# Optimization experiments

Hardware: AMD Instinct MI355X
Metric: run time of the kernel (lower is better)

Reference implementation:

```python
import jax, jax.numpy as jnp
import numpy as np

B, T, F, H, V = 16, 512, 512, 2048, 64
INPUT_INT_SCALE = 3.0
INT16_MIN, INT16_MAX = -32768, 32767


def setup_inputs() -> dict:
    key = jax.random.key(0)
    ks = jax.random.split(key, 8)
    x = jax.random.normal(ks[0], (B, T, F), dtype=jnp.float32)
    # int4 weights stored as int32 in [-8, 7]
    W_res_i4 = jax.random.randint(ks[1], (H, H), -8, 8, dtype=jnp.int32)
    W_in_i4 = jax.random.randint(ks[2], (H, F), -8, 8, dtype=jnp.int32)
    # per-row quantization scales (positive)
    S_res_row = jax.random.uniform(ks[3], (H,), dtype=jnp.float32, minval=0.01, maxval=0.2)
    S_in_row = jax.random.uniform(ks[4], (H,), dtype=jnp.float32, minval=0.01, maxval=0.2)
    g_res = jnp.float32(1.0)
    g_in = jnp.float32(1.0)
    W_out_w = jax.random.normal(ks[5], (V, H), dtype=jnp.float32) / np.float32(np.sqrt(H))
    W_out_b = jnp.zeros((V,), dtype=jnp.float32)
    return {
        "x": x, "S_res_row": S_res_row, "S_in_row": S_in_row,
        "g_res": g_res, "g_in": g_in,
        "W_out_w": W_out_w, "W_out_b": W_out_b,
        "W_res_i4": W_res_i4, "W_in_i4": W_in_i4,
    }


def reference(x, S_res_row, S_in_row, g_res, g_in, W_out_w, W_out_b, W_res_i4, W_in_i4):
    # row scales (matches _row_scales)
    s_res = (S_res_row / 49.0 * g_res)[None, :]                     # (1,H)
    s_in = (S_in_row / (7.0 * max(1.0, INPUT_INT_SCALE)) * g_in)[None, :]  # (1,H)

    def step(h, x_t):
        # quantize input frame and hidden state to integers (detached in torch)
        u_int = jax.lax.stop_gradient(jnp.round(x_t * INPUT_INT_SCALE)).astype(jnp.int32)     # (B,F)
        h_int = jax.lax.stop_gradient(jnp.round(jnp.clip(h, -1.0, 1.0) * 7.0)).astype(jnp.int32)  # (B,H)
        # integer matvecs: y[b,k] = sum_j W[k,j] * v[b,j]
        out_res = jnp.einsum('bh,kh->bk', h_int, W_res_i4)  # (B,H) int32
        out_in = jnp.einsum('bf,kf->bk', u_int, W_in_i4)    # (B,H) int32
        # int16 saturation, then row scale + gain, tanh
        out_res_f = jnp.clip(out_res, INT16_MIN, INT16_MAX).astype(jnp.float32)
        out_in_f = jnp.clip(out_in, INT16_MIN, INT16_MAX).astype(jnp.float32)
        h_new = jnp.tanh(out_res_f * s_res + out_in_f * s_in)
        return h_new, h_new

    h0 = jnp.zeros((x.shape[0], W_res_i4.shape[0]), dtype=jnp.float32)
    _, Hs = jax.lax.scan(step, h0, jnp.swapaxes(x, 0, 1))  # (T,B,H)
    Hs = jnp.swapaxes(Hs, 0, 1)                            # (B,T,H)
    # readout
    return jnp.einsum('bth,vh->btv', Hs, W_out_w) + W_out_b
```

## Files before the change

### kernel.cpp

```cpp
#include <hip/hip_runtime.h>
#include <hip/hip_bf16.h>


#define B_ 16
#define T_ 512
#define F_ 512
#define H_ 2048
#define V_ 64
#define SLICES 16
#define RPW 128
#define NTHREADS 256
#define NWG 256

#if defined(__has_builtin)
#if __has_builtin(__builtin_amdgcn_sdot8)
#define HAVE_SDOT8 1
#endif
#endif

__device__ __forceinline__ int sdot8(int a, int b, int c) {
#ifdef HAVE_SDOT8
  return __builtin_amdgcn_sdot8(a, b, c, false);
#else
#pragma unroll
  for (int i = 0; i < 8; ++i) {
    int av = (a << (28 - 4 * i)) >> 28;
    int bv = (b << (28 - 4 * i)) >> 28;
    c += av * bv;
  }
  return c;
#endif
}

__device__ __forceinline__ float tanh_ref(float x) {
  float ax = fabsf(x);
  float xc = fminf(fmaxf(x, -7.90531110763549805f), 7.90531110763549805f);
  float x2 = __fmul_rn(xc, xc);
  float p = -2.76076847742355e-16f;
  p = __fmaf_rn(x2, p, 2.00018790482477e-13f);
  p = __fmaf_rn(x2, p, -8.60467152213735e-11f);
  p = __fmaf_rn(x2, p, 5.12229709037114e-08f);
  p = __fmaf_rn(x2, p, 1.48572235717979e-05f);
  p = __fmaf_rn(x2, p, 6.37261928875436e-04f);
  p = __fmaf_rn(x2, p, 4.89352455891786e-03f);
  p = __fmul_rn(xc, p);
  float q = 1.19825839466702e-06f;
  q = __fmaf_rn(x2, q, 1.18534705686654e-04f);
  q = __fmaf_rn(x2, q, 2.26843463243900e-03f);
  q = __fmaf_rn(x2, q, 4.89352518554385e-03f);
  float r = __fdiv_rn(p, q);
  return (ax < 0.0004f) ? x : r;
}

__device__ __forceinline__ unsigned f2bf(float f) {
  unsigned u = __float_as_uint(f);
  return (u + 0x7fffu + ((u >> 16) & 1u)) >> 16;
}

__device__ __forceinline__ unsigned poll_tag(const unsigned long long* p, unsigned tag) {
  unsigned long long u;
  do {
    u = __hip_atomic_load(p, __ATOMIC_RELAXED, __HIP_MEMORY_SCOPE_AGENT);
  } while ((unsigned)(u >> 32) != tag);
  return (unsigned)u;
}

__device__ __forceinline__ void publish_tag(unsigned long long* p, unsigned data, unsigned tag) {
  unsigned long long u = ((unsigned long long)tag << 32) | data;
  __hip_atomic_store(p, u, __ATOMIC_RELAXED, __HIP_MEMORY_SCOPE_AGENT);
}

__global__ void pack_weights(const int* __restrict__ Wres, const int* __restrict__ Win,
                             int* __restrict__ wr4, int* __restrict__ wi4) {
  int id = blockIdx.x * blockDim.x + threadIdx.x;
  if (id < H_ * 256) {
    const int* src = Wres + id * 8;
    int pk = 0;
#pragma unroll
    for (int i = 0; i < 8; ++i) pk |= (src[i] & 15) << (4 * i);
    wr4[id] = pk;
  } else {
    int id2 = id - H_ * 256;
    if (id2 < H_ * 64) {
      const int* src = Win + id2 * 8;
      int pk = 0;
#pragma unroll
      for (int i = 0; i < 8; ++i) pk |= (src[i] & 15) << (4 * i);
      wi4[id2] = pk;
    }
  }
}

__global__ void pack_u(const float* __restrict__ x, int* __restrict__ um, int* __restrict__ ua) {
  int idx = blockIdx.x * blockDim.x + threadIdx.x;
  if (idx >= B_ * T_ * 64) return;
  const float* src = x + (size_t)idx * 8;
  int pm = 0, pa = 0;
#pragma unroll
  for (int i = 0; i < 8; ++i) {
    int u = (int)rintf(__fmul_rn(src[i], 3.0f));
    int vv = u + 128;
    pm |= (vv & 7) << (4 * i);
    pa |= (((vv >> 3) - 16) & 15) << (4 * i);
  }
  um[idx] = pm;
  ua[idx] = pa;
}

__global__ void __launch_bounds__(NTHREADS, 1) esn_main(
    const int* __restrict__ um, const int* __restrict__ ua,
    const int* __restrict__ wr4, const int* __restrict__ wi4,
    unsigned long long* hq2,
    const float* __restrict__ S_res, const float* __restrict__ S_in,
    const float* __restrict__ g_res, const float* __restrict__ g_in,
    unsigned* __restrict__ Hs, int t0, int t1) {
  extern __shared__ char smem[];
  ::int4* lw4 = (::int4*)smem;
  int* lds_h4 = (int*)(lw4 + 8192);
  int* lds_um = lds_h4 + 256;
  int* lds_ua = lds_um + 64;

  const int wg = blockIdx.x;
  const int b = wg & 15, slice = wg >> 4;
  const int tid = threadIdx.x;
  const unsigned lane = tid & 63;
  const int wave = tid >> 6;
  const int half = tid & 1;
  const int grow = slice * RPW + (tid >> 1);

  {
    const ::int4* gw = (const ::int4*)wr4;
#pragma unroll 4
    for (int m = 0; m < 32; ++m) lw4[m * 256 + tid] = gw[grow * 64 + half * 32 + m];
  }
  ::int4 rwm[8];
  {
    const ::int4* gwi = (const ::int4*)wi4;
#pragma unroll
    for (int m = 0; m < 8; ++m) rwm[m] = gwi[grow * 16 + half * 8 + m];
  }
  const float sr = __fmul_rn(__fdiv_rn(S_res[grow], 49.0f), g_res[0]);
  const float si = __fmul_rn(__fdiv_rn(S_in[grow], 21.0f), g_in[0]);

  const ::int4* lh4 = (const ::int4*)lds_h4 + half * 32;
  const ::int4* lum4 = (const ::int4*)lds_um + half * 8;
  const ::int4* lua4 = (const ::int4*)lds_ua + half * 8;

  unsigned ureg = 0;
  if (tid < 64)
    ureg = um[(b * T_ + t0) * 64 + tid];
  else if (tid < 128)
    ureg = ua[(b * T_ + t0) * 64 + (tid - 64)];

  for (int t = t0; t < t1; ++t) {
    const int cur = t & 1, nxt = cur ^ 1;
    if (tid < 64)
      lds_um[tid] = ureg;
    else if (tid < 128)
      lds_ua[tid - 64] = ureg;
    __syncthreads();

    unsigned unext = 0;
    if (t + 1 < t1) {
      if (tid < 64)
        unext = um[(b * T_ + t + 1) * 64 + tid];
      else if (tid < 128)
        unext = ua[(b * T_ + t + 1) * 64 + (tid - 64)];
    }

    int am = 0, aa = 0;
#pragma unroll
    for (int m = 0; m < 8; ++m) {
      ::int4 w = rwm[m];
      ::int4 uM = lum4[m];
      ::int4 uA = lua4[m];
      am = sdot8(w.x, uM.x, am); am = sdot8(w.y, uM.y, am);
      am = sdot8(w.z, uM.z, am); am = sdot8(w.w, uM.w, am);
      aa = sdot8(w.x, uA.x, aa); aa = sdot8(w.y, uA.y, aa);
      aa = sdot8(w.z, uA.z, aa); aa = sdot8(w.w, uA.w, aa);
    }
    int accin = am + (aa << 3);
    accin += __shfl_xor(accin, 1);

    unsigned hd = poll_tag(hq2 + ((size_t)(cur * 16 + b) * 256 + tid), (unsigned)t);
    lds_h4[tid] = (int)hd;
    __syncthreads();

    int c0 = 0, c1 = 0, c2 = 0, c3 = 0;
#pragma unroll
    for (int m = 0; m < 32; m += 4) {
      ::int4 w0 = lw4[(m + 0) * 256 + tid];
      ::int4 w1 = lw4[(m + 1) * 256 + tid];
      ::int4 w2 = lw4[(m + 2) * 256 + tid];
      ::int4 w3 = lw4[(m + 3) * 256 + tid];
      ::int4 h0 = lh4[m + 0];
      ::int4 h1 = lh4[m + 1];
      ::int4 h2 = lh4[m + 2];
      ::int4 h3 = lh4[m + 3];
      c0 = sdot8(w0.x, h0.x, c0); c0 = sdot8(w0.y, h0.y, c0);
      c0 = sdot8(w0.z, h0.z, c0); c0 = sdot8(w0.w, h0.w, c0);
      c1 = sdot8(w1.x, h1.x, c1); c1 = sdot8(w1.y, h1.y, c1);
      c1 = sdot8(w1.z, h1.z, c1); c1 = sdot8(w1.w, h1.w, c1);
      c2 = sdot8(w2.x, h2.x, c2); c2 = sdot8(w2.y, h2.y, c2);
      c2 = sdot8(w2.z, h2.z, c2); c2 = sdot8(w2.w, h2.w, c2);
      c3 = sdot8(w3.x, h3.x, c3); c3 = sdot8(w3.y, h3.y, c3);
      c3 = sdot8(w3.z, h3.z, c3); c3 = sdot8(w3.w, h3.w, c3);
    }
    int acc = (c0 + c1) + (c2 + c3);
    acc += __shfl_xor(acc, 1);

    int cr = min(max(acc, -32768), 32767);
    int ci = min(max(accin, -32768), 32767);
    float arg = __fadd_rn(__fmul_rn((float)cr, sr), __fmul_rn((float)ci, si));
    float hn = tanh_ref(arg);
    float hc = fminf(fmaxf(hn, -1.0f), 1.0f);
    int qv = (int)rintf(__fmul_rn(hc, 7.0f));

    unsigned nib = ((unsigned)qv & 15u) << (4 * ((lane >> 1) & 7));
    nib |= (unsigned)__shfl_xor((int)nib, 1);
    nib |= (unsigned)__shfl_xor((int)nib, 2);
    nib |= (unsigned)__shfl_xor((int)nib, 4);
    nib |= (unsigned)__shfl_xor((int)nib, 8);
    if ((lane & 15) == 0)
      publish_tag(hq2 + ((size_t)(nxt * 16 + b) * 256 + slice * 16 + wave * 4 + (lane >> 4)),
                  nib, (unsigned)(t + 1));

    unsigned bfb = f2bf(hn);
    unsigned other = (unsigned)__shfl_xor((int)bfb, 2);
    if ((tid & 3) == 0)
      Hs[(size_t)(b * T_ + t) * (H_ / 2) + slice * 64 + (tid >> 2)] = bfb | (other << 16);

    ureg = unext;
  }
}

#define ACC8(acc, p, w0, w1)                                    \
  acc = fmaf(__uint_as_float(p.x << 16), w0.x, acc);            \
  acc = fmaf(__uint_as_float(p.x & 0xffff0000u), w0.y, acc);    \
  acc = fmaf(__uint_as_float(p.y << 16), w0.z, acc);            \
  acc = fmaf(__uint_as_float(p.y & 0xffff0000u), w0.w, acc);    \
  acc = fmaf(__uint_as_float(p.z << 16), w1.x, acc);            \
  acc = fmaf(__uint_as_float(p.z & 0xffff0000u), w1.y, acc);    \
  acc = fmaf(__uint_as_float(p.w << 16), w1.z, acc);            \
  acc = fmaf(__uint_as_float(p.w & 0xffff0000u), w1.w, acc);

__global__ void __launch_bounds__(256) readout(const unsigned* __restrict__ Hs,
                                               const float* __restrict__ Wout,
                                               const float* __restrict__ Wb,
                                               float* __restrict__ out) {
  const int v = threadIdx.x & 63;
  const int rg = threadIdx.x >> 6;
  const int bt0 = blockIdx.x * 16 + rg * 4;
  const float* wrow = Wout + (size_t)v * H_;
  const unsigned* h0 = Hs + (size_t)bt0 * (H_ / 2);
  float a0 = Wb[v], a1 = a0, a2 = a0, a3 = a0;
  for (int j = 0; j < H_ / 2; j += 4) {
    float4 w0 = *(const float4*)(wrow + 2 * j);
    float4 w1 = *(const float4*)(wrow + 2 * j + 4);
    uint4 p0 = *(const uint4*)(h0 + j);
    uint4 p1 = *(const uint4*)(h0 + (H_ / 2) + j);
    uint4 p2 = *(const uint4*)(h0 + 2 * (H_ / 2) + j);
    uint4 p3 = *(const uint4*)(h0 + 3 * (H_ / 2) + j);
    ACC8(a0, p0, w0, w1)
    ACC8(a1, p1, w0, w1)
    ACC8(a2, p2, w0, w1)
    ACC8(a3, p3, w0, w1)
  }
  out[(size_t)(bt0 + 0) * V_ + v] = a0;
  out[(size_t)(bt0 + 1) * V_ + v] = a1;
  out[(size_t)(bt0 + 2) * V_ + v] = a2;
  out[(size_t)(bt0 + 3) * V_ + v] = a3;
}

extern "C" void kernel_launch(void* const* d_in, const int* in_sizes, int n_in,
                              void* d_out, int out_size, void* d_ws, size_t ws_size,
                              hipStream_t stream) {
  const float* x = (const float*)d_in[0];
  const float* S_res = (const float*)d_in[1];
  const float* S_in = (const float*)d_in[2];
  const float* g_res = (const float*)d_in[3];
  const float* g_in = (const float*)d_in[4];
  const float* Woutw = (const float*)d_in[5];
  const float* Woutb = (const float*)d_in[6];
  const int* Wres = (const int*)d_in[7];
  const int* Win = (const int*)d_in[8];

  char* ws = (char*)d_ws;
  unsigned long long* hq2 = (unsigned long long*)(ws + 4096);
  int* um = (int*)(ws + (1 << 20));
  int* ua = um + (1 << 19);
  int* wr4 = ua + (1 << 19);
  int* wi4 = wr4 + (1 << 19);
  unsigned* Hs = (unsigned*)(ws + (8 << 20));

  hipMemsetAsync(d_ws, 0, 4096 + 65536, stream);
  hipLaunchKernelGGL(pack_weights, dim3(2560), dim3(256), 0, stream, Wres, Win, wr4, wi4);
  hipLaunchKernelGGL(pack_u, dim3(2048), dim3(256), 0, stream, x, um, ua);

  const int smem_bytes = 131072 + 1536;
  (void)hipFuncSetAttribute((const void*)esn_main, hipFuncAttributeMaxDynamicSharedMemorySize,
                            smem_bytes);

  float* outf = (float*)d_out;
  int t0 = 0, t1 = T_;
  void* args[] = {&um, &ua, &wr4, &wi4, &hq2, &S_res, &S_in,
                  &g_res, &g_in, &Hs, &t0, &t1};
  hipError_t e = hipLaunchCooperativeKernel((const void*)esn_main, dim3(NWG), dim3(NTHREADS),
                                            args, smem_bytes, stream);
  if (e != hipSuccess) {
    for (int t = 0; t < T_; ++t) {
      hipLaunchKernelGGL(esn_main, dim3(NWG), dim3(NTHREADS), smem_bytes, stream,
                         um, ua, wr4, wi4, hq2, S_res, S_in, g_res, g_in, Hs, t, t + 1);
    }
  }
  hipLaunchKernelGGL(readout, dim3(B_ * T_ / 16), dim3(256), 0, stream,
                     Hs, Woutw, Woutb, outf);
}
```

Measured before the change: 1.118 ms.

## Split recurrent matvec across 512 workgroups with four threads per row

Raises the workgroup count from 256 to 512, so each block owns 64 hidden rows and four threads share a row (quarter-K each), halving per-block LDS weight footprint and allowing two blocks per CU. The hidden-state poll is now done by one wave reading four tagged words per lane with s_sleep backoff, written into a padded, double-buffered LDS array, which removes one barrier per step. Weight LDS reads are issued early via inline asm ds_read_b128 before the poll so they overlap the wait, and the next input frame is prefetched two steps ahead. The cost is more blocks polling and publishing through global memory per step, plus extra shuffle reductions.

```diff
diff --git a/kernel.cpp b/kernel.cpp
--- a/kernel.cpp
+++ b/kernel.cpp
@@ -7,10 +7,12 @@
 #define F_ 512
 #define H_ 2048
 #define V_ 64
-#define SLICES 16
-#define RPW 128
+#define SLICES 32
+#define RPW 64
 #define NTHREADS 256
-#define NWG 256
+#define NWG 512
+
+typedef int i4v __attribute__((ext_vector_type(4)));
 
 #if defined(__has_builtin)
 #if __has_builtin(__builtin_amdgcn_sdot8)
@@ -57,14 +59,6 @@
   return (u + 0x7fffu + ((u >> 16) & 1u)) >> 16;
 }
 
-__device__ __forceinline__ unsigned poll_tag(const unsigned long long* p, unsigned tag) {
-  unsigned long long u;
-  do {
-    u = __hip_atomic_load(p, __ATOMIC_RELAXED, __HIP_MEMORY_SCOPE_AGENT);
-  } while ((unsigned)(u >> 32) != tag);
-  return (unsigned)u;
-}
-
 __device__ __forceinline__ void publish_tag(unsigned long long* p, unsigned data, unsigned tag) {
   unsigned long long u = ((unsigned long long)tag << 32) | data;
   __hip_atomic_store(p, u, __ATOMIC_RELAXED, __HIP_MEMORY_SCOPE_AGENT);
@@ -107,107 +101,127 @@
   ua[idx] = pa;
 }
 
-__global__ void __launch_bounds__(NTHREADS, 1) esn_main(
+#define WLD(i, OFFSTR) \
+  asm volatile("ds_read_b128 %0, %1 offset:" OFFSTR : "=v"(wreg[i]) : "v"(lds_wb))
+
+__global__ void __launch_bounds__(NTHREADS, 2) esn_main(
     const int* __restrict__ um, const int* __restrict__ ua,
     const int* __restrict__ wr4, const int* __restrict__ wi4,
     unsigned long long* hq2,
     const float* __restrict__ S_res, const float* __restrict__ S_in,
     const float* __restrict__ g_res, const float* __restrict__ g_in,
     unsigned* __restrict__ Hs, int t0, int t1) {
-  extern __shared__ char smem[];
+  extern __shared__ __align__(16) char smem[];
   ::int4* lw4 = (::int4*)smem;
-  int* lds_h4 = (int*)(lw4 + 8192);
-  int* lds_um = lds_h4 + 256;
-  int* lds_ua = lds_um + 64;
+  int* lds_h = (int*)(lw4 + 16 * 256);
+  int* lds_u = lds_h + 2 * 272;
 
   const int wg = blockIdx.x;
   const int b = wg & 15, slice = wg >> 4;
   const int tid = threadIdx.x;
   const unsigned lane = tid & 63;
-  const int wave = tid >> 6;
-  const int half = tid & 1;
-  const int grow = slice * RPW + (tid >> 1);
+  const int q = tid & 3;
+  const int grow = slice * RPW + (tid >> 2);
 
   {
     const ::int4* gw = (const ::int4*)wr4;
 #pragma unroll 4
-    for (int m = 0; m < 32; ++m) lw4[m * 256 + tid] = gw[grow * 64 + half * 32 + m];
-  }
-  ::int4 rwm[8];
+    for (int m = 0; m < 16; ++m) lw4[m * 256 + tid] = gw[grow * 64 + q * 16 + m];
+  }
+  ::int4 rwm[4];
   {
     const ::int4* gwi = (const ::int4*)wi4;
 #pragma unroll
-    for (int m = 0; m < 8; ++m) rwm[m] = gwi[grow * 16 + half * 8 + m];
+    for (int m = 0; m < 4; ++m) rwm[m] = gwi[grow * 16 + q * 4 + m];
   }
   const float sr = __fmul_rn(__fdiv_rn(S_res[grow], 49.0f), g_res[0]);
   const float si = __fmul_rn(__fdiv_rn(S_in[grow], 21.0f), g_in[0]);
 
-  const ::int4* lh4 = (const ::int4*)lds_h4 + half * 32;
-  const ::int4* lum4 = (const ::int4*)lds_um + half * 8;
-  const ::int4* lua4 = (const ::int4*)lds_ua + half * 8;
+  const unsigned lds_wb = (unsigned)(size_t)smem + (unsigned)tid * 16u;
 
   unsigned ureg = 0;
-  if (tid < 64)
-    ureg = um[(b * T_ + t0) * 64 + tid];
-  else if (tid < 128)
-    ureg = ua[(b * T_ + t0) * 64 + (tid - 64)];
+  if (tid < 128) {
+    unsigned v0 = (tid < 64) ? (unsigned)um[(b * T_ + t0) * 64 + tid]
+                             : (unsigned)ua[(b * T_ + t0) * 64 + (tid - 64)];
+    lds_u[(t0 & 1) * 128 + tid] = (int)v0;
+    if (t0 + 1 < T_)
+      ureg = (tid < 64) ? (unsigned)um[(b * T_ + t0 + 1) * 64 + tid]
+                        : (unsigned)ua[(b * T_ + t0 + 1) * 64 + (tid - 64)];
+  }
+  __syncthreads();
 
   for (int t = t0; t < t1; ++t) {
-    const int cur = t & 1, nxt = cur ^ 1;
-    if (tid < 64)
-      lds_um[tid] = ureg;
-    else if (tid < 128)
-      lds_ua[tid - 64] = ureg;
-    __syncthreads();
-
-    unsigned unext = 0;
-    if (t + 1 < t1) {
-      if (tid < 64)
-        unext = um[(b * T_ + t + 1) * 64 + tid];
-      else if (tid < 128)
-        unext = ua[(b * T_ + t + 1) * 64 + (tid - 64)];
-    }
+    const int cbuf = t & 1, nbuf = cbuf ^ 1;
+    if (t + 1 < t1 && tid < 128) lds_u[nbuf * 128 + tid] = (int)ureg;
 
     int am = 0, aa = 0;
-#pragma unroll
-    for (int m = 0; m < 8; ++m) {
-      ::int4 w = rwm[m];
-      ::int4 uM = lum4[m];
-      ::int4 uA = lua4[m];
-      am = sdot8(w.x, uM.x, am); am = sdot8(w.y, uM.y, am);
-      am = sdot8(w.z, uM.z, am); am = sdot8(w.w, uM.w, am);
-      aa = sdot8(w.x, uA.x, aa); aa = sdot8(w.y, uA.y, aa);
-      aa = sdot8(w.z, uA.z, aa); aa = sdot8(w.w, uA.w, aa);
+    {
+      const ::int4* lu = (const ::int4*)(lds_u + cbuf * 128);
+#pragma unroll
+      for (int m = 0; m < 4; ++m) {
+        ::int4 w = rwm[m];
+        ::int4 uM = lu[q * 4 + m];
+        ::int4 uA = lu[16 + q * 4 + m];
+        am = sdot8(w.x, uM.x, am); am = sdot8(w.y, uM.y, am);
+        am = sdot8(w.z, uM.z, am); am = sdot8(w.w, uM.w, am);
+        aa = sdot8(w.x, uA.x, aa); aa = sdot8(w.y, uA.y, aa);
+        aa = sdot8(w.z, uA.z, aa); aa = sdot8(w.w, uA.w, aa);
+      }
     }
     int accin = am + (aa << 3);
     accin += __shfl_xor(accin, 1);
-
-    unsigned hd = poll_tag(hq2 + ((size_t)(cur * 16 + b) * 256 + tid), (unsigned)t);
-    lds_h4[tid] = (int)hd;
+    accin += __shfl_xor(accin, 2);
+
+    i4v wreg[16];
+    WLD(0, "0");      WLD(1, "4096");   WLD(2, "8192");   WLD(3, "12288");
+    WLD(4, "16384");  WLD(5, "20480");  WLD(6, "24576");  WLD(7, "28672");
+    WLD(8, "32768");  WLD(9, "36864");  WLD(10, "40960"); WLD(11, "45056");
+    WLD(12, "49152"); WLD(13, "53248"); WLD(14, "57344"); WLD(15, "61440");
+
+    if (tid < 64) {
+      const unsigned long long* p = hq2 + (size_t)(cbuf * 16 + b) * 256 + tid * 4;
+      unsigned long long u0, u1, u2, u3;
+      const unsigned tag = (unsigned)t;
+      for (;;) {
+        u0 = __hip_atomic_load(p + 0, __ATOMIC_RELAXED, __HIP_MEMORY_SCOPE_AGENT);
+        u1 = __hip_atomic_load(p + 1, __ATOMIC_RELAXED, __HIP_MEMORY_SCOPE_AGENT);
+        u2 = __hip_atomic_load(p + 2, __ATOMIC_RELAXED, __HIP_MEMORY_SCOPE_AGENT);
+        u3 = __hip_atomic_load(p + 3, __ATOMIC_RELAXED, __HIP_MEMORY_SCOPE_AGENT);
+        unsigned d = ((unsigned)(u0 >> 32) ^ tag) | ((unsigned)(u1 >> 32) ^ tag) |
+                     ((unsigned)(u2 >> 32) ^ tag) | ((unsigned)(u3 >> 32) ^ tag);
+        if (d == 0) break;
+        __builtin_amdgcn_s_sleep(1);
+      }
+      ::int4 hv;
+      hv.x = (int)u0; hv.y = (int)u1; hv.z = (int)u2; hv.w = (int)u3;
+      ((::int4*)(lds_h + cbuf * 272))[(tid >> 4) * 17 + (tid & 15)] = hv;
+    }
+
     __syncthreads();
+    __builtin_amdgcn_sched_barrier(0);
 
     int c0 = 0, c1 = 0, c2 = 0, c3 = 0;
-#pragma unroll
-    for (int m = 0; m < 32; m += 4) {
-      ::int4 w0 = lw4[(m + 0) * 256 + tid];
-      ::int4 w1 = lw4[(m + 1) * 256 + tid];
-      ::int4 w2 = lw4[(m + 2) * 256 + tid];
-      ::int4 w3 = lw4[(m + 3) * 256 + tid];
-      ::int4 h0 = lh4[m + 0];
-      ::int4 h1 = lh4[m + 1];
-      ::int4 h2 = lh4[m + 2];
-      ::int4 h3 = lh4[m + 3];
-      c0 = sdot8(w0.x, h0.x, c0); c0 = sdot8(w0.y, h0.y, c0);
-      c0 = sdot8(w0.z, h0.z, c0); c0 = sdot8(w0.w, h0.w, c0);
-      c1 = sdot8(w1.x, h1.x, c1); c1 = sdot8(w1.y, h1.y, c1);
-      c1 = sdot8(w1.z, h1.z, c1); c1 = sdot8(w1.w, h1.w, c1);
-      c2 = sdot8(w2.x, h2.x, c2); c2 = sdot8(w2.y, h2.y, c2);
-      c2 = sdot8(w2.z, h2.z, c2); c2 = sdot8(w2.w, h2.w, c2);
-      c3 = sdot8(w3.x, h3.x, c3); c3 = sdot8(w3.y, h3.y, c3);
-      c3 = sdot8(w3.z, h3.z, c3); c3 = sdot8(w3.w, h3.w, c3);
+    {
+      const ::int4* lh = (const ::int4*)(lds_h + cbuf * 272);
+#pragma unroll
+      for (int m = 0; m < 16; m += 4) {
+        ::int4 h0 = lh[q * 17 + m + 0];
+        ::int4 h1 = lh[q * 17 + m + 1];
+        ::int4 h2 = lh[q * 17 + m + 2];
+        ::int4 h3 = lh[q * 17 + m + 3];
+        c0 = sdot8(wreg[m + 0].x, h0.x, c0); c0 = sdot8(wreg[m + 0].y, h0.y, c0);
+        c0 = sdot8(wreg[m + 0].z, h0.z, c0); c0 = sdot8(wreg[m + 0].w, h0.w, c0);
+        c1 = sdot8(wreg[m + 1].x, h1.x, c1); c1 = sdot8(wreg[m + 1].y, h1.y, c1);
+        c1 = sdot8(wreg[m + 1].z, h1.z, c1); c1 = sdot8(wreg[m + 1].w, h1.w, c1);
+        c2 = sdot8(wreg[m + 2].x, h2.x, c2); c2 = sdot8(wreg[m + 2].y, h2.y, c2);
+        c2 = sdot8(wreg[m + 2].z, h2.z, c2); c2 = sdot8(wreg[m + 2].w, h2.w, c2);
+        c3 = sdot8(wreg[m + 3].x, h3.x, c3); c3 = sdot8(wreg[m + 3].y, h3.y, c3);
+        c3 = sdot8(wreg[m + 3].z, h3.z, c3); c3 = sdot8(wreg[m + 3].w, h3.w, c3);
+      }
     }
     int acc = (c0 + c1) + (c2 + c3);
     acc += __shfl_xor(acc, 1);
+    acc += __shfl_xor(acc, 2);
 
     int cr = min(max(acc, -32768), 32767);
     int ci = min(max(accin, -32768), 32767);
@@ -216,21 +230,22 @@
     float hc = fminf(fmaxf(hn, -1.0f), 1.0f);
     int qv = (int)rintf(__fmul_rn(hc, 7.0f));
 
-    unsigned nib = ((unsigned)qv & 15u) << (4 * ((lane >> 1) & 7));
-    nib |= (unsigned)__shfl_xor((int)nib, 1);
-    nib |= (unsigned)__shfl_xor((int)nib, 2);
+    unsigned nib = ((unsigned)qv & 15u) << (4 * ((lane >> 2) & 7));
     nib |= (unsigned)__shfl_xor((int)nib, 4);
     nib |= (unsigned)__shfl_xor((int)nib, 8);
-    if ((lane & 15) == 0)
-      publish_tag(hq2 + ((size_t)(nxt * 16 + b) * 256 + slice * 16 + wave * 4 + (lane >> 4)),
+    nib |= (unsigned)__shfl_xor((int)nib, 16);
+    if ((lane & 31) == 0)
+      publish_tag(hq2 + (size_t)((t ^ 1) & 1) * 0 +
+                      (size_t)(nbuf * 16 + b) * 256 + slice * 8 + (tid >> 6) * 2 + (lane >> 5),
                   nib, (unsigned)(t + 1));
 
     unsigned bfb = f2bf(hn);
-    unsigned other = (unsigned)__shfl_xor((int)bfb, 2);
-    if ((tid & 3) == 0)
-      Hs[(size_t)(b * T_ + t) * (H_ / 2) + slice * 64 + (tid >> 2)] = bfb | (other << 16);
-
-    ureg = unext;
+    unsigned other = (unsigned)__shfl_xor((int)bfb, 4);
+    if ((tid & 7) == 0)
+      Hs[(size_t)(b * T_ + t) * (H_ / 2) + slice * 32 + (tid >> 3)] = bfb | (other << 16);
+    if (t + 2 < T_ && tid < 128)
+      ureg = (tid < 64) ? (unsigned)um[(b * T_ + t + 2) * 64 + tid]
+                        : (unsigned)ua[(b * T_ + t + 2) * 64 + (tid - 64)];
   }
 }
 
@@ -297,11 +312,10 @@
   hipLaunchKernelGGL(pack_weights, dim3(2560), dim3(256), 0, stream, Wres, Win, wr4, wi4);
   hipLaunchKernelGGL(pack_u, dim3(2048), dim3(256), 0, stream, x, um, ua);
 
-  const int smem_bytes = 131072 + 1536;
+  const int smem_bytes = 65536 + 2 * 272 * 4 + 2 * 128 * 4;
   (void)hipFuncSetAttribute((const void*)esn_main, hipFuncAttributeMaxDynamicSharedMemorySize,
                             smem_bytes);
 
-  float* outf = (float*)d_out;
   int t0 = 0, t1 = T_;
   void* args[] = {&um, &ua, &wr4, &wi4, &hq2, &S_res, &S_in,
                   &g_res, &g_in, &Hs, &t0, &t1};
@@ -314,5 +328,5 @@
     }
   }
   hipLaunchKernelGGL(readout, dim3(B_ * T_ / 16), dim3(256), 0, stream,
-                     Hs, Woutw, Woutb, outf);
-}
+                     Hs, Woutw, Woutb, (float*)d_out);
+}
```

After: 1.040 ms. 1.07x faster.

## Hoist input projection into batched GEMM and restructure recurrence with replicated flags

Applied to the files above, without the earlier changes.

Computes the input projection for all timesteps in a separate parallel kernel before the recurrence, removing it from the serial critical path. The recurrent kernel is reorganized so each workgroup owns 8 rows across all batches. Each wave handles one batch per step and keeps its weights in registers instead of LDS. Hidden-state nibbles are published to REP replicated flag buffers to spread polling contention, and the next steps' flag loads are software-prefetched so the pipeline runs four steps deep. This adds an fp32 intermediate buffer of B*T*H and a multi-copy store per step.

```diff
diff --git a/kernel.cpp b/kernel.cpp
--- a/kernel.cpp
+++ b/kernel.cpp
@@ -7,10 +7,11 @@
 #define F_ 512
 #define H_ 2048
 #define V_ 64
-#define SLICES 16
-#define RPW 128
-#define NTHREADS 256
 #define NWG 256
+#define NTHREADS 128
+#define REP 8
+
+typedef unsigned long long ull;
 
 #if defined(__has_builtin)
 #if __has_builtin(__builtin_amdgcn_sdot8)
@@ -57,17 +58,11 @@
   return (u + 0x7fffu + ((u >> 16) & 1u)) >> 16;
 }
 
-__device__ __forceinline__ unsigned poll_tag(const unsigned long long* p, unsigned tag) {
-  unsigned long long u;
-  do {
-    u = __hip_atomic_load(p, __ATOMIC_RELAXED, __HIP_MEMORY_SCOPE_AGENT);
-  } while ((unsigned)(u >> 32) != tag);
-  return (unsigned)u;
-}
-
-__device__ __forceinline__ void publish_tag(unsigned long long* p, unsigned data, unsigned tag) {
-  unsigned long long u = ((unsigned long long)tag << 32) | data;
-  __hip_atomic_store(p, u, __ATOMIC_RELAXED, __HIP_MEMORY_SCOPE_AGENT);
+__device__ __forceinline__ ull xld(const ull* p) {
+  return __hip_atomic_load(p, __ATOMIC_RELAXED, __HIP_MEMORY_SCOPE_AGENT);
+}
+__device__ __forceinline__ void xst(ull* p, ull v) {
+  __hip_atomic_store(p, v, __ATOMIC_RELAXED, __HIP_MEMORY_SCOPE_AGENT);
 }
 
 __global__ void pack_weights(const int* __restrict__ Wres, const int* __restrict__ Win,
@@ -107,131 +102,158 @@
   ua[idx] = pa;
 }
 
+__global__ void __launch_bounds__(256) input_gemm(
+    const int* __restrict__ um, const int* __restrict__ ua, const int* __restrict__ wi4,
+    const float* __restrict__ S_in, const float* __restrict__ g_in, float* __restrict__ fin) {
+  __shared__ int su[1024];
+  const int btg = blockIdx.x;
+  const int row = blockIdx.y * 256 + threadIdx.x;
+  for (int k = threadIdx.x; k < 1024; k += 256) {
+    int bt = k >> 7, c = k & 127;
+    su[k] = (c < 64) ? um[(btg * 8 + bt) * 64 + c] : ua[(btg * 8 + bt) * 64 + (c - 64)];
+  }
+  __syncthreads();
+  ::int4 w[16];
+  const ::int4* gw = (const ::int4*)wi4;
+#pragma unroll
+  for (int i = 0; i < 16; ++i) w[i] = gw[row * 16 + i];
+  const float si = __fmul_rn(__fdiv_rn(S_in[row], 21.0f), g_in[0]);
+#pragma unroll
+  for (int g = 0; g < 8; ++g) {
+    const ::int4* uM = (const ::int4*)(su + g * 128);
+    const ::int4* uA = (const ::int4*)(su + g * 128 + 64);
+    int am = 0, aa = 0;
+#pragma unroll
+    for (int i = 0; i < 16; ++i) {
+      ::int4 wi = w[i]; ::int4 m = uM[i]; ::int4 a = uA[i];
+      am = sdot8(wi.x, m.x, am); am = sdot8(wi.y, m.y, am);
+      am = sdot8(wi.z, m.z, am); am = sdot8(wi.w, m.w, am);
+      aa = sdot8(wi.x, a.x, aa); aa = sdot8(wi.y, a.y, aa);
+      aa = sdot8(wi.z, a.z, aa); aa = sdot8(wi.w, a.w, aa);
+    }
+    int acc = am + (aa << 3);
+    acc = min(max(acc, -32768), 32767);
+    fin[(size_t)(btg * 8 + g) * H_ + row] = __fmul_rn((float)acc, si);
+  }
+}
+
 __global__ void __launch_bounds__(NTHREADS, 1) esn_main(
-    const int* __restrict__ um, const int* __restrict__ ua,
-    const int* __restrict__ wr4, const int* __restrict__ wi4,
-    unsigned long long* hq2,
-    const float* __restrict__ S_res, const float* __restrict__ S_in,
-    const float* __restrict__ g_res, const float* __restrict__ g_in,
-    unsigned* __restrict__ Hs, int t0, int t1) {
-  extern __shared__ char smem[];
-  ::int4* lw4 = (::int4*)smem;
-  int* lds_h4 = (int*)(lw4 + 8192);
-  int* lds_um = lds_h4 + 256;
-  int* lds_ua = lds_um + 64;
-
+    const int* __restrict__ wr4, ull* hq,
+    const float* __restrict__ S_res, const float* __restrict__ g_res,
+    const float* __restrict__ fin, unsigned* __restrict__ Hs, int t0, int t1) {
+  __shared__ int lds_h[2][320];
   const int wg = blockIdx.x;
-  const int b = wg & 15, slice = wg >> 4;
   const int tid = threadIdx.x;
-  const unsigned lane = tid & 63;
-  const int wave = tid >> 6;
-  const int half = tid & 1;
-  const int grow = slice * RPW + (tid >> 1);
-
+  const int wv = tid >> 6;
+  const int lane = tid & 63;
+  const int r = lane >> 3, kq = lane & 7;
+  const int grow = wg * 8 + r;
+  const size_t cpy = (size_t)(wg & (REP - 1));
+  int* hb = lds_h[wv];
+  const int wofs = (lane >> 2) * 20 + (lane & 3) * 4;
+  int* hrd = hb + 40 * kq;
+
+  ::int4 wreg[8];
   {
     const ::int4* gw = (const ::int4*)wr4;
-#pragma unroll 4
-    for (int m = 0; m < 32; ++m) lw4[m * 256 + tid] = gw[grow * 64 + half * 32 + m];
-  }
-  ::int4 rwm[8];
-  {
-    const ::int4* gwi = (const ::int4*)wi4;
-#pragma unroll
-    for (int m = 0; m < 8; ++m) rwm[m] = gwi[grow * 16 + half * 8 + m];
+#pragma unroll
+    for (int j = 0; j < 8; ++j) wreg[j] = gw[grow * 64 + kq * 8 + j];
   }
   const float sr = __fmul_rn(__fdiv_rn(S_res[grow], 49.0f), g_res[0]);
-  const float si = __fmul_rn(__fdiv_rn(S_in[grow], 21.0f), g_in[0]);
-
-  const ::int4* lh4 = (const ::int4*)lds_h4 + half * 32;
-  const ::int4* lum4 = (const ::int4*)lds_um + half * 8;
-  const ::int4* lua4 = (const ::int4*)lds_ua + half * 8;
-
-  unsigned ureg = 0;
-  if (tid < 64)
-    ureg = um[(b * T_ + t0) * 64 + tid];
-  else if (tid < 128)
-    ureg = ua[(b * T_ + t0) * 64 + (tid - 64)];
-
-  for (int t = t0; t < t1; ++t) {
-    const int cur = t & 1, nxt = cur ^ 1;
-    if (tid < 64)
-      lds_um[tid] = ureg;
-    else if (tid < 128)
-      lds_ua[tid - 64] = ureg;
-    __syncthreads();
-
-    unsigned unext = 0;
-    if (t + 1 < t1) {
-      if (tid < 64)
-        unext = um[(b * T_ + t + 1) * 64 + tid];
-      else if (tid < 128)
-        unext = ua[(b * T_ + t + 1) * 64 + (tid - 64)];
-    }
-
-    int am = 0, aa = 0;
-#pragma unroll
-    for (int m = 0; m < 8; ++m) {
-      ::int4 w = rwm[m];
-      ::int4 uM = lum4[m];
-      ::int4 uA = lua4[m];
-      am = sdot8(w.x, uM.x, am); am = sdot8(w.y, uM.y, am);
-      am = sdot8(w.z, uM.z, am); am = sdot8(w.w, uM.w, am);
-      aa = sdot8(w.x, uA.x, aa); aa = sdot8(w.y, uA.y, aa);
-      aa = sdot8(w.z, uA.z, aa); aa = sdot8(w.w, uA.w, aa);
-    }
-    int accin = am + (aa << 3);
-    accin += __shfl_xor(accin, 1);
-
-    unsigned hd = poll_tag(hq2 + ((size_t)(cur * 16 + b) * 256 + tid), (unsigned)t);
-    lds_h4[tid] = (int)hd;
-    __syncthreads();
-
-    int c0 = 0, c1 = 0, c2 = 0, c3 = 0;
-#pragma unroll
-    for (int m = 0; m < 32; m += 4) {
-      ::int4 w0 = lw4[(m + 0) * 256 + tid];
-      ::int4 w1 = lw4[(m + 1) * 256 + tid];
-      ::int4 w2 = lw4[(m + 2) * 256 + tid];
-      ::int4 w3 = lw4[(m + 3) * 256 + tid];
-      ::int4 h0 = lh4[m + 0];
-      ::int4 h1 = lh4[m + 1];
-      ::int4 h2 = lh4[m + 2];
-      ::int4 h3 = lh4[m + 3];
-      c0 = sdot8(w0.x, h0.x, c0); c0 = sdot8(w0.y, h0.y, c0);
-      c0 = sdot8(w0.z, h0.z, c0); c0 = sdot8(w0.w, h0.w, c0);
-      c1 = sdot8(w1.x, h1.x, c1); c1 = sdot8(w1.y, h1.y, c1);
-      c1 = sdot8(w1.z, h1.z, c1); c1 = sdot8(w1.w, h1.w, c1);
-      c2 = sdot8(w2.x, h2.x, c2); c2 = sdot8(w2.y, h2.y, c2);
-      c2 = sdot8(w2.z, h2.z, c2); c2 = sdot8(w2.w, h2.w, c2);
-      c3 = sdot8(w3.x, h3.x, c3); c3 = sdot8(w3.y, h3.y, c3);
-      c3 = sdot8(w3.z, h3.z, c3); c3 = sdot8(w3.w, h3.w, c3);
-    }
-    int acc = (c0 + c1) + (c2 + c3);
-    acc += __shfl_xor(acc, 1);
-
-    int cr = min(max(acc, -32768), 32767);
-    int ci = min(max(accin, -32768), 32767);
-    float arg = __fadd_rn(__fmul_rn((float)cr, sr), __fmul_rn((float)ci, si));
-    float hn = tanh_ref(arg);
-    float hc = fminf(fmaxf(hn, -1.0f), 1.0f);
-    int qv = (int)rintf(__fmul_rn(hc, 7.0f));
-
-    unsigned nib = ((unsigned)qv & 15u) << (4 * ((lane >> 1) & 7));
-    nib |= (unsigned)__shfl_xor((int)nib, 1);
-    nib |= (unsigned)__shfl_xor((int)nib, 2);
-    nib |= (unsigned)__shfl_xor((int)nib, 4);
-    nib |= (unsigned)__shfl_xor((int)nib, 8);
-    if ((lane & 15) == 0)
-      publish_tag(hq2 + ((size_t)(nxt * 16 + b) * 256 + slice * 16 + wave * 4 + (lane >> 4)),
-                  nib, (unsigned)(t + 1));
-
-    unsigned bfb = f2bf(hn);
-    unsigned other = (unsigned)__shfl_xor((int)bfb, 2);
-    if ((tid & 3) == 0)
-      Hs[(size_t)(b * T_ + t) * (H_ / 2) + slice * 64 + (tid >> 2)] = bfb | (other << 16);
-
-    ureg = unext;
-  }
+
+  const int sBeg = t0 * 8, sEnd = t1 * 8;
+
+#define PRE(P, sarg)                                                                     \
+  {                                                                                      \
+    int sc_ = (sarg);                                                                    \
+    if (sc_ > sEnd - 1) sc_ = sEnd - 1;                                                  \
+    const int tt_ = sc_ >> 3, bb_ = ((sc_ & 7) << 1) | wv;                               \
+    const ull* pp_ = hq + (((cpy << 5) + ((size_t)(tt_ & 1) << 4) + bb_) << 8) + (lane << 2); \
+    P##a = xld(pp_); P##b = xld(pp_ + 1); P##c = xld(pp_ + 2); P##d = xld(pp_ + 3);      \
+    P##f = fin[((((size_t)bb_ << 9) + tt_) << 11) + grow];                               \
+  }
+
+#define CONS(P, sarg)                                                                    \
+  {                                                                                      \
+    const int s_ = (sarg);                                                               \
+    const int tt = s_ >> 3;                                                              \
+    const int bb = ((s_ & 7) << 1) | wv;                                                 \
+    const unsigned tg = (unsigned)tt;                                                    \
+    const ull* pp = hq + (((cpy << 5) + ((size_t)(tt & 1) << 4) + bb) << 8) + (lane << 2); \
+    while ((((unsigned)(P##a >> 32)) ^ tg) | (((unsigned)(P##b >> 32)) ^ tg) |           \
+           (((unsigned)(P##c >> 32)) ^ tg) | (((unsigned)(P##d >> 32)) ^ tg)) {          \
+      P##a = xld(pp); P##b = xld(pp + 1); P##c = xld(pp + 2); P##d = xld(pp + 3);        \
+    }                                                                                    \
+    ::int4 hv_;                                                                          \
+    hv_.x = (int)P##a; hv_.y = (int)P##b; hv_.z = (int)P##c; hv_.w = (int)P##d;          \
+    const float finv = P##f;                                                             \
+    PRE(P, s_ + 4);                                                                      \
+    *(::int4*)(hb + wofs) = hv_;                                                         \
+    __builtin_amdgcn_sched_barrier(0);                                                   \
+    int c0 = 0, c1 = 0, c2 = 0, c3 = 0;                                                  \
+    {                                                                                    \
+      ::int4 h0 = *(const ::int4*)(hrd + 0);  ::int4 h1 = *(const ::int4*)(hrd + 4);     \
+      ::int4 h2 = *(const ::int4*)(hrd + 8);  ::int4 h3 = *(const ::int4*)(hrd + 12);    \
+      ::int4 h4 = *(const ::int4*)(hrd + 20); ::int4 h5 = *(const ::int4*)(hrd + 24);    \
+      ::int4 h6 = *(const ::int4*)(hrd + 28); ::int4 h7 = *(const ::int4*)(hrd + 32);    \
+      c0 = sdot8(wreg[0].x, h0.x, c0); c0 = sdot8(wreg[0].y, h0.y, c0);                  \
+      c0 = sdot8(wreg[0].z, h0.z, c0); c0 = sdot8(wreg[0].w, h0.w, c0);                  \
+      c1 = sdot8(wreg[1].x, h1.x, c1); c1 = sdot8(wreg[1].y, h1.y, c1);                  \
+      c1 = sdot8(wreg[1].z, h1.z, c1); c1 = sdot8(wreg[1].w, h1.w, c1);                  \
+      c2 = sdot8(wreg[2].x, h2.x, c2); c2 = sdot8(wreg[2].y, h2.y, c2);                  \
+      c2 = sdot8(wreg[2].z, h2.z, c2); c2 = sdot8(wreg[2].w, h2.w, c2);                  \
+      c3 = sdot8(wreg[3].x, h3.x, c3); c3 = sdot8(wreg[3].y, h3.y, c3);                  \
+      c3 = sdot8(wreg[3].z, h3.z, c3); c3 = sdot8(wreg[3].w, h3.w, c3);                  \
+      c0 = sdot8(wreg[4].x, h4.x, c0); c0 = sdot8(wreg[4].y, h4.y, c0);                  \
+      c0 = sdot8(wreg[4].z, h4.z, c0); c0 = sdot8(wreg[4].w, h4.w, c0);                  \
+      c1 = sdot8(wreg[5].x, h5.x, c1); c1 = sdot8(wreg[5].y, h5.y, c1);                  \
+      c1 = sdot8(wreg[5].z, h5.z, c1); c1 = sdot8(wreg[5].w, h5.w, c1);                  \
+      c2 = sdot8(wreg[6].x, h6.x, c2); c2 = sdot8(wreg[6].y, h6.y, c2);                  \
+      c2 = sdot8(wreg[6].z, h6.z, c2); c2 = sdot8(wreg[6].w, h6.w, c2);                  \
+      c3 = sdot8(wreg[7].x, h7.x, c3); c3 = sdot8(wreg[7].y, h7.y, c3);                  \
+      c3 = sdot8(wreg[7].z, h7.z, c3); c3 = sdot8(wreg[7].w, h7.w, c3);                  \
+    }                                                                                    \
+    int acc = (c0 + c1) + (c2 + c3);                                                     \
+    acc += __shfl_xor(acc, 1);                                                           \
+    acc += __shfl_xor(acc, 2);                                                           \
+    acc += __shfl_xor(acc, 4);                                                           \
+    int cr = min(max(acc, -32768), 32767);                                               \
+    float arg = __fadd_rn(__fmul_rn((float)cr, sr), finv);                               \
+    float hn = tanh_ref(arg);                                                            \
+    float hc = fminf(fmaxf(hn, -1.0f), 1.0f);                                            \
+    int qv = (int)rintf(__fmul_rn(hc, 7.0f));                                            \
+    unsigned nib = ((unsigned)qv & 15u) << (4 * r);                                      \
+    nib |= (unsigned)__shfl_xor((int)nib, 8);                                            \
+    nib |= (unsigned)__shfl_xor((int)nib, 16);                                           \
+    nib |= (unsigned)__shfl_xor((int)nib, 32);                                           \
+    if (lane == 0) {                                                                     \
+      ull uv = ((ull)(unsigned)(tt + 1) << 32) | nib;                                    \
+      ull* pb = hq + ((((size_t)((tt + 1) & 1) << 4) + bb) << 8) + wg;                   \
+      _Pragma("unroll")                                                                  \
+      for (int c_ = 0; c_ < REP; ++c_) xst(pb + ((size_t)c_ << 13), uv);                 \
+    }                                                                                    \
+    unsigned bfb = f2bf(hn);                                                             \
+    unsigned oth = (unsigned)__shfl_xor((int)bfb, 8);                                    \
+    if ((lane & 15) == 0)                                                                \
+      Hs[((((size_t)bb << 9) + tt) << 10) + wg * 4 + (lane >> 4)] = bfb | (oth << 16);   \
+  }
+
+  ull p0a, p0b, p0c, p0d; float p0f;
+  ull p1a, p1b, p1c, p1d; float p1f;
+  ull p2a, p2b, p2c, p2d; float p2f;
+  ull p3a, p3b, p3c, p3d; float p3f;
+  PRE(p0, sBeg)
+  PRE(p1, sBeg + 1)
+  PRE(p2, sBeg + 2)
+  PRE(p3, sBeg + 3)
+  for (int s = sBeg; s < sEnd; s += 4) {
+    CONS(p0, s)
+    CONS(p1, s + 1)
+    CONS(p2, s + 2)
+    CONS(p3, s + 3)
+  }
+#undef PRE
+#undef CONS
 }
 
 #define ACC8(acc, p, w0, w1)                                    \
@@ -286,33 +308,30 @@
   const int* Win = (const int*)d_in[8];
 
   char* ws = (char*)d_ws;
-  unsigned long long* hq2 = (unsigned long long*)(ws + 4096);
-  int* um = (int*)(ws + (1 << 20));
-  int* ua = um + (1 << 19);
-  int* wr4 = ua + (1 << 19);
-  int* wi4 = wr4 + (1 << 19);
-  unsigned* Hs = (unsigned*)(ws + (8 << 20));
-
-  hipMemsetAsync(d_ws, 0, 4096 + 65536, stream);
+  ull* hq = (ull*)ws;
+  int* wr4 = (int*)(ws + (1 << 20));
+  int* wi4 = (int*)(ws + (3 << 20));
+  int* um = (int*)(ws + ((size_t)4 << 20));
+  int* ua = (int*)(ws + ((size_t)6 << 20));
+  unsigned* Hs = (unsigned*)(ws + ((size_t)8 << 20));
+  float* fin = (float*)(ws + ((size_t)40 << 20));
+
+  hipMemsetAsync(hq, 0, (size_t)REP * 32 * 256 * 8, stream);
   hipLaunchKernelGGL(pack_weights, dim3(2560), dim3(256), 0, stream, Wres, Win, wr4, wi4);
   hipLaunchKernelGGL(pack_u, dim3(2048), dim3(256), 0, stream, x, um, ua);
-
-  const int smem_bytes = 131072 + 1536;
-  (void)hipFuncSetAttribute((const void*)esn_main, hipFuncAttributeMaxDynamicSharedMemorySize,
-                            smem_bytes);
-
-  float* outf = (float*)d_out;
+  hipLaunchKernelGGL(input_gemm, dim3(B_ * T_ / 8, 8), dim3(256), 0, stream,
+                     um, ua, wi4, S_in, g_in, fin);
+
   int t0 = 0, t1 = T_;
-  void* args[] = {&um, &ua, &wr4, &wi4, &hq2, &S_res, &S_in,
-                  &g_res, &g_in, &Hs, &t0, &t1};
+  void* args[] = {&wr4, &hq, &S_res, &g_res, &fin, &Hs, &t0, &t1};
   hipError_t e = hipLaunchCooperativeKernel((const void*)esn_main, dim3(NWG), dim3(NTHREADS),
-                                            args, smem_bytes, stream);
+                                            args, 0, stream);
   if (e != hipSuccess) {
     for (int t = 0; t < T_; ++t) {
-      hipLaunchKernelGGL(esn_main, dim3(NWG), dim3(NTHREADS), smem_bytes, stream,
-                         um, ua, wr4, wi4, hq2, S_res, S_in, g_res, g_in, Hs, t, t + 1);
+      hipLaunchKernelGGL(esn_main, dim3(NWG), dim3(NTHREADS), 0, stream,
+                         wr4, hq, S_res, g_res, fin, Hs, t, t + 1);
     }
   }
   hipLaunchKernelGGL(readout, dim3(B_ * T_ / 16), dim3(256), 0, stream,
-                     Hs, Woutw, Woutb, outf);
-}
+                     Hs, Woutw, Woutb, (float*)d_out);
+}
```

Result: slower. 3.401 ms (+204.2%).
